# Performance work log

Hardware: AMD Instinct MI355X
Metric: run time of the kernel (lower is better)

Reference implementation:

```python
import jax, jax.numpy as jnp
import numpy as np

DIM_IN = 1024
DIM_OUT = 1024
BATCH = 4
SEQ = 2048


def setup_inputs() -> dict:
    key = jax.random.key(0)
    kx, kq, kk, kv = jax.random.split(key, 4)
    scale = 1.0 / np.sqrt(DIM_IN)
    x = jax.random.normal(kx, (BATCH, SEQ, DIM_IN), dtype=jnp.float32)
    # Weights stored as [dim_in, dim_out] (transpose of torch Linear's [out, in]);
    # y = x @ W is equivalent math to torch's x @ W_t.T
    Wq = jax.random.normal(kq, (DIM_IN, DIM_OUT), dtype=jnp.float32) * scale
    Wk = jax.random.normal(kk, (DIM_IN, DIM_OUT), dtype=jnp.float32) * scale
    Wv = jax.random.normal(kv, (DIM_IN, DIM_OUT), dtype=jnp.float32) * scale
    return {"x": x, "Wq": Wq, "Wk": Wk, "Wv": Wv}


def reference(x, Wq, Wk, Wv):
    # x: [b, s, d_in]; single-head causal self-attention (dropout=0 -> identity)
    q = jnp.einsum("bsd,de->bse", x, Wq)
    k = jnp.einsum("bsd,de->bse", x, Wk)
    v = jnp.einsum("bsd,de->bse", x, Wv)
    dim_k = k.shape[-1]
    scores = jnp.einsum("bqe,bke->bqk", q, k) / jnp.sqrt(jnp.float32(dim_k))
    s = x.shape[1]
    causal = jnp.tril(jnp.ones((s, s), dtype=bool))  # True = keep
    scores = jnp.where(causal[None, :, :], scores, -jnp.inf)
    weights = jax.nn.softmax(scores, axis=-1)
    context = jnp.einsum("bqk,bke->bqe", weights, v)
    return context
```

## Files before the change

### kernel.cpp

```cpp
#include <hip/hip_runtime.h>
#include <cstdint>
#include <cstddef>

typedef unsigned short u16;
typedef __bf16 bf16x8 __attribute__((ext_vector_type(8)));
typedef float f32x4 __attribute__((ext_vector_type(4)));

__device__ inline u16 f2b(float f) {
    uint32_t u = __builtin_bit_cast(uint32_t, f);
    u += 0x7FFFu + ((u >> 16) & 1u);
    return (u16)(u >> 16);
}

__device__ inline void gl2lds16(const u16* g, u16* l) {
    __builtin_amdgcn_global_load_lds(
        (const __attribute__((address_space(1))) void*)g,
        (__attribute__((address_space(3))) void*)l, 16, 0, 0);
}

__global__ void convert_x_kernel(const float* __restrict__ x, u16* __restrict__ xb) {
    size_t i = ((size_t)blockIdx.x * 256 + threadIdx.x) * 4;
    float4 v = *(const float4*)(x + i);
    uint2 pack;
    pack.x = (uint32_t)f2b(v.x) | ((uint32_t)f2b(v.y) << 16);
    pack.y = (uint32_t)f2b(v.z) | ((uint32_t)f2b(v.w) << 16);
    *(uint2*)(xb + i) = pack;
}

__global__ void transpose_w_kernel(const float* __restrict__ Wq,
                                   const float* __restrict__ Wk,
                                   const float* __restrict__ Wv,
                                   u16* __restrict__ QKWT, u16* __restrict__ WvT) {
    __shared__ u16 t[32][33];
    const int z = blockIdx.z;
    const float* W = (z == 0) ? Wq : ((z == 1) ? Wk : Wv);
    u16* dst = (z == 0) ? QKWT : ((z == 1) ? QKWT + 1024 * 1024 : WvT);
    const float scale = (z == 0) ? 0.03125f : 1.0f;
    const int bx = blockIdx.x * 32;
    const int by = blockIdx.y * 32;
    const int tx = threadIdx.x, ty = threadIdx.y;
    #pragma unroll
    for (int r = 0; r < 32; r += 8)
        t[ty + r][tx] = f2b(W[(size_t)(by + ty + r) * 1024 + bx + tx] * scale);
    __syncthreads();
    #pragma unroll
    for (int r = 0; r < 32; r += 8)
        dst[(size_t)(bx + ty + r) * 1024 + (by + tx)] = t[tx][ty + r];
}

template<int EPI>
__device__ __forceinline__ void gemm_body(
    u16* __restrict__ smem,
    const u16* __restrict__ A, int lda,
    const u16* __restrict__ B, int ldb,
    char* __restrict__ Cb, int ldc,
    int m0, int n0, int Kloc, float* __restrict__ lrow) {
    constexpr int BK = 32;
    const int tid = threadIdx.x;
    const int lane = tid & 63, wave = tid >> 6;
    const int wm = wave >> 1, wn = wave & 1;
    const int fl = lane & 15, fh = lane >> 4;

    const int q0 = wave * 2;
    const int srow = lane >> 2, skoff = (lane & 3) * 8;
    const u16* ApL0 = A + (size_t)(m0 + q0 * 16 + srow) * lda + skoff;
    const u16* ApL1 = ApL0 + (size_t)16 * lda;
    const u16* BpL0 = B + (size_t)(n0 + q0 * 16 + srow) * ldb + skoff;
    const u16* BpL1 = BpL0 + (size_t)16 * ldb;

    u16* const Ab[2] = { smem, smem + 4096 };
    u16* const Bb[2] = { smem + 8192, smem + 12288 };

    auto issue = [&](int buf, int k0) {
        gl2lds16(ApL0 + k0, Ab[buf] + q0 * 512);
        gl2lds16(ApL1 + k0, Ab[buf] + q0 * 512 + 512);
        gl2lds16(BpL0 + k0, Bb[buf] + q0 * 512);
        gl2lds16(BpL1 + k0, Bb[buf] + q0 * 512 + 512);
    };

    const f32x4 vzero = {0.f, 0.f, 0.f, 0.f};
    f32x4 acc[4][4];
    #pragma unroll
    for (int i = 0; i < 4; ++i)
        #pragma unroll
        for (int j = 0; j < 4; ++j) acc[i][j] = vzero;

    issue(0, 0);
    int buf = 0;
    for (int k0 = 0; k0 < Kloc; k0 += BK, buf ^= 1) {
        __syncthreads();
        if (k0 + BK < Kloc) issue(buf ^ 1, k0 + BK);
        bf16x8 af[4], bfr[4];
        #pragma unroll
        for (int t = 0; t < 4; ++t) {
            af[t]  = *(const bf16x8*)&Ab[buf][(wm * 64 + t * 16 + fl) * BK + fh * 8];
            bfr[t] = *(const bf16x8*)&Bb[buf][(wn * 64 + t * 16 + fl) * BK + fh * 8];
        }
        #pragma unroll
        for (int mt = 0; mt < 4; ++mt)
            #pragma unroll
            for (int nt = 0; nt < 4; ++nt)
                acc[mt][nt] = __builtin_amdgcn_mfma_f32_16x16x32_bf16(
                    af[mt], bfr[nt], acc[mt][nt], 0, 0, 0);
    }

    if (EPI == 0) {
        u16* Cp = (u16*)Cb;
        #pragma unroll
        for (int mt = 0; mt < 4; ++mt)
            #pragma unroll
            for (int nt = 0; nt < 4; ++nt)
                #pragma unroll
                for (int r = 0; r < 4; ++r) {
                    int row = m0 + wm * 64 + mt * 16 + fh * 4 + r;
                    int col = n0 + wn * 64 + nt * 16 + fl;
                    Cp[(size_t)row * ldc + col] = f2b(acc[mt][nt][r]);
                }
    } else if (EPI == 2) {
        u16* Cp = (u16*)Cb;
        #pragma unroll
        for (int mt = 0; mt < 4; ++mt)
            #pragma unroll
            for (int r = 0; r < 4; ++r) {
                int row = m0 + wm * 64 + mt * 16 + fh * 4 + r;
                float part = 0.f;
                #pragma unroll
                for (int nt = 0; nt < 4; ++nt) {
                    int col = n0 + wn * 64 + nt * 16 + fl;
                    float p = (col <= row) ? __expf(acc[mt][nt][r]) : 0.f;
                    part += p;
                    Cp[(size_t)row * ldc + col] = f2b(p);
                }
                #pragma unroll
                for (int off = 1; off < 16; off <<= 1)
                    part += __shfl_xor(part, off, 64);
                if (fl == 0) atomicAdd(lrow + row, part);
            }
    } else {
        float* Cp = (float*)Cb;
        #pragma unroll
        for (int mt = 0; mt < 4; ++mt)
            #pragma unroll
            for (int r = 0; r < 4; ++r) {
                int row = m0 + wm * 64 + mt * 16 + fh * 4 + r;
                float inv = 1.0f / lrow[row];
                #pragma unroll
                for (int nt = 0; nt < 4; ++nt) {
                    int col = n0 + wn * 64 + nt * 16 + fl;
                    Cp[(size_t)row * ldc + col] = acc[mt][nt][r] * inv;
                }
            }
    }
}

__global__ __launch_bounds__(256)
void proj_kernel(const u16* __restrict__ xb, const u16* __restrict__ QKWT,
                 const u16* __restrict__ WvT, u16* __restrict__ QK,
                 u16* __restrict__ Vt) {
    __shared__ __align__(16) u16 smem[16384];
    int bid = blockIdx.x;
    const u16 *A, *B;
    char* C;
    int lda, ldb, ldc, m0, n0;
    if (bid < 1024) {
        int jt = bid & 15, it = bid >> 4;
        A = xb;  lda = 1024;  B = QKWT;  ldb = 1024;
        C = (char*)QK;  ldc = 2048;  m0 = it * 128;  n0 = jt * 128;
    } else {
        int b = bid - 1024;
        int jt = b & 63, it = b >> 6;
        A = WvT;  lda = 1024;  B = xb;  ldb = 1024;
        C = (char*)Vt;  ldc = 8192;  m0 = it * 128;  n0 = jt * 128;
    }
    gemm_body<0>(smem, A, lda, B, ldb, C, ldc, m0, n0, 1024, nullptr);
}

__global__ __launch_bounds__(256)
void scores_kernel(const u16* __restrict__ QK, u16* __restrict__ P,
                   float* __restrict__ l) {
    __shared__ __align__(16) u16 smem[16384];
    const int t = blockIdx.x, z = blockIdx.y;
    int it = (int)((sqrtf(8.0f * t + 1.0f) - 1.0f) * 0.5f);
    while ((it + 1) * (it + 2) / 2 <= t) ++it;
    while (it * (it + 1) / 2 > t) --it;
    const int jt = t - it * (it + 1) / 2;
    const u16* Qz = QK + (size_t)z * 2048 * 2048;
    const u16* Kz = Qz + 1024;
    u16* Pz = P + (size_t)z * 2048 * 2048;
    gemm_body<2>(smem, Qz, 2048, Kz, 2048, (char*)Pz, 2048,
                 it * 128, jt * 128, 1024, l + (size_t)z * 2048);
}

__global__ __launch_bounds__(256)
void out_kernel(const u16* __restrict__ P, const u16* __restrict__ Vt,
                float* __restrict__ out, float* __restrict__ l) {
    __shared__ __align__(16) u16 smem[16384];
    const int jt = blockIdx.x;
    const int it = 15 - (int)blockIdx.y;
    const int z = blockIdx.z;
    gemm_body<3>(smem, P + (size_t)z * 2048 * 2048, 2048,
                 Vt + (size_t)z * 2048, 8192,
                 (char*)(out + (size_t)z * 2048 * 1024), 1024,
                 it * 128, jt * 128, (it + 1) * 128, l + (size_t)z * 2048);
}

extern "C" void kernel_launch(void* const* d_in, const int* in_sizes, int n_in,
                              void* d_out, int out_size, void* d_ws, size_t ws_size,
                              hipStream_t stream) {
    (void)in_sizes; (void)n_in; (void)out_size; (void)ws_size;
    const float* x  = (const float*)d_in[0];
    const float* Wq = (const float*)d_in[1];
    const float* Wk = (const float*)d_in[2];
    const float* Wv = (const float*)d_in[3];
    float* out = (float*)d_out;

    const size_t MB = 1u << 20;
    char* ws = (char*)d_ws;
    u16* xb   = (u16*)(ws);
    u16* QKWT = (u16*)(ws + 16 * MB);
    u16* WvT  = (u16*)(ws + 20 * MB);
    u16* QK   = (u16*)(ws + 22 * MB);
    u16* Vt   = (u16*)(ws + 54 * MB);
    u16* P    = (u16*)(ws + 70 * MB);
    float* l  = (float*)(ws + 102 * MB);

    hipMemsetAsync(l, 0, 8192 * sizeof(float), stream);
    convert_x_kernel<<<8192, 256, 0, stream>>>(x, xb);
    transpose_w_kernel<<<dim3(32, 32, 3), dim3(32, 8), 0, stream>>>(Wq, Wk, Wv, QKWT, WvT);

    proj_kernel<<<1536, 256, 0, stream>>>(xb, QKWT, WvT, QK, Vt);
    scores_kernel<<<dim3(136, 4), 256, 0, stream>>>(QK, P, l);
    out_kernel<<<dim3(8, 16, 4), 256, 0, stream>>>(P, Vt, out, l);
}
```

Measured before the change: 257.6 us.

## Replace LDS-staged GEMM tiles with direct register-prefetched global loads

The shared GEMM body stops staging A/B tiles through LDS with global_load_lds double buffering and barriers. Each wave now loads its MFMA fragments straight from global memory into registers, software-pipelined two K-steps deep, and launch bounds request 3 blocks per SM. This removes LDS traffic and __syncthreads, but gives up data sharing across waves: each tile is fetched twice from global/L2, and register pressure rises. Out_kernel's K length, (it+1)*128, is a multiple of 64, so the unrolled-by-64 loop stays valid.

Measured after the change: 483.2 us. 87.6% more time.

```diff
diff --git a/kernel.cpp b/kernel.cpp
--- a/kernel.cpp
+++ b/kernel.cpp
@@ -10,12 +10,6 @@
     uint32_t u = __builtin_bit_cast(uint32_t, f);
     u += 0x7FFFu + ((u >> 16) & 1u);
     return (u16)(u >> 16);
-}
-
-__device__ inline void gl2lds16(const u16* g, u16* l) {
-    __builtin_amdgcn_global_load_lds(
-        (const __attribute__((address_space(1))) void*)g,
-        (__attribute__((address_space(3))) void*)l, 16, 0, 0);
 }
 
 __global__ void convert_x_kernel(const float* __restrict__ x, u16* __restrict__ xb) {
@@ -50,33 +44,19 @@
 
 template<int EPI>
 __device__ __forceinline__ void gemm_body(
-    u16* __restrict__ smem,
     const u16* __restrict__ A, int lda,
     const u16* __restrict__ B, int ldb,
     char* __restrict__ Cb, int ldc,
     int m0, int n0, int Kloc, float* __restrict__ lrow) {
-    constexpr int BK = 32;
     const int tid = threadIdx.x;
     const int lane = tid & 63, wave = tid >> 6;
     const int wm = wave >> 1, wn = wave & 1;
     const int fl = lane & 15, fh = lane >> 4;
 
-    const int q0 = wave * 2;
-    const int srow = lane >> 2, skoff = (lane & 3) * 8;
-    const u16* ApL0 = A + (size_t)(m0 + q0 * 16 + srow) * lda + skoff;
-    const u16* ApL1 = ApL0 + (size_t)16 * lda;
-    const u16* BpL0 = B + (size_t)(n0 + q0 * 16 + srow) * ldb + skoff;
-    const u16* BpL1 = BpL0 + (size_t)16 * ldb;
-
-    u16* const Ab[2] = { smem, smem + 4096 };
-    u16* const Bb[2] = { smem + 8192, smem + 12288 };
-
-    auto issue = [&](int buf, int k0) {
-        gl2lds16(ApL0 + k0, Ab[buf] + q0 * 512);
-        gl2lds16(ApL1 + k0, Ab[buf] + q0 * 512 + 512);
-        gl2lds16(BpL0 + k0, Bb[buf] + q0 * 512);
-        gl2lds16(BpL1 + k0, Bb[buf] + q0 * 512 + 512);
-    };
+    const u16* Ap = A + (size_t)(m0 + wm * 64 + fl) * lda + fh * 8;
+    const u16* Bp = B + (size_t)(n0 + wn * 64 + fl) * ldb + fh * 8;
+    const size_t sA = (size_t)16 * lda;
+    const size_t sB = (size_t)16 * ldb;
 
     const f32x4 vzero = {0.f, 0.f, 0.f, 0.f};
     f32x4 acc[4][4];
@@ -85,23 +65,39 @@
         #pragma unroll
         for (int j = 0; j < 4; ++j) acc[i][j] = vzero;
 
-    issue(0, 0);
-    int buf = 0;
-    for (int k0 = 0; k0 < Kloc; k0 += BK, buf ^= 1) {
-        __syncthreads();
-        if (k0 + BK < Kloc) issue(buf ^ 1, k0 + BK);
-        bf16x8 af[4], bfr[4];
+    bf16x8 a0[4], b0[4], a1[4], b1[4];
+
+    #pragma unroll
+    for (int t = 0; t < 4; ++t) {
+        a0[t] = *(const bf16x8*)(Ap + t * sA);
+        b0[t] = *(const bf16x8*)(Bp + t * sB);
+    }
+
+    for (int k0 = 0; k0 < Kloc; k0 += 64) {
         #pragma unroll
         for (int t = 0; t < 4; ++t) {
-            af[t]  = *(const bf16x8*)&Ab[buf][(wm * 64 + t * 16 + fl) * BK + fh * 8];
-            bfr[t] = *(const bf16x8*)&Bb[buf][(wn * 64 + t * 16 + fl) * BK + fh * 8];
+            a1[t] = *(const bf16x8*)(Ap + t * sA + k0 + 32);
+            b1[t] = *(const bf16x8*)(Bp + t * sB + k0 + 32);
         }
         #pragma unroll
         for (int mt = 0; mt < 4; ++mt)
             #pragma unroll
             for (int nt = 0; nt < 4; ++nt)
                 acc[mt][nt] = __builtin_amdgcn_mfma_f32_16x16x32_bf16(
-                    af[mt], bfr[nt], acc[mt][nt], 0, 0, 0);
+                    a0[mt], b0[nt], acc[mt][nt], 0, 0, 0);
+        if (k0 + 64 < Kloc) {
+            #pragma unroll
+            for (int t = 0; t < 4; ++t) {
+                a0[t] = *(const bf16x8*)(Ap + t * sA + k0 + 64);
+                b0[t] = *(const bf16x8*)(Bp + t * sB + k0 + 64);
+            }
+        }
+        #pragma unroll
+        for (int mt = 0; mt < 4; ++mt)
+            #pragma unroll
+            for (int nt = 0; nt < 4; ++nt)
+                acc[mt][nt] = __builtin_amdgcn_mfma_f32_16x16x32_bf16(
+                    a1[mt], b1[nt], acc[mt][nt], 0, 0, 0);
     }
 
     if (EPI == 0) {
@@ -153,32 +149,26 @@
     }
 }
 
-__global__ __launch_bounds__(256)
+__global__ __launch_bounds__(256, 3)
 void proj_kernel(const u16* __restrict__ xb, const u16* __restrict__ QKWT,
                  const u16* __restrict__ WvT, u16* __restrict__ QK,
                  u16* __restrict__ Vt) {
-    __shared__ __align__(16) u16 smem[16384];
     int bid = blockIdx.x;
-    const u16 *A, *B;
-    char* C;
-    int lda, ldb, ldc, m0, n0;
     if (bid < 1024) {
         int jt = bid & 15, it = bid >> 4;
-        A = xb;  lda = 1024;  B = QKWT;  ldb = 1024;
-        C = (char*)QK;  ldc = 2048;  m0 = it * 128;  n0 = jt * 128;
+        gemm_body<0>(xb, 1024, QKWT, 1024, (char*)QK, 2048,
+                     it * 128, jt * 128, 1024, nullptr);
     } else {
         int b = bid - 1024;
         int jt = b & 63, it = b >> 6;
-        A = WvT;  lda = 1024;  B = xb;  ldb = 1024;
-        C = (char*)Vt;  ldc = 8192;  m0 = it * 128;  n0 = jt * 128;
-    }
-    gemm_body<0>(smem, A, lda, B, ldb, C, ldc, m0, n0, 1024, nullptr);
-}
-
-__global__ __launch_bounds__(256)
+        gemm_body<0>(WvT, 1024, xb, 1024, (char*)Vt, 8192,
+                     it * 128, jt * 128, 1024, nullptr);
+    }
+}
+
+__global__ __launch_bounds__(256, 3)
 void scores_kernel(const u16* __restrict__ QK, u16* __restrict__ P,
                    float* __restrict__ l) {
-    __shared__ __align__(16) u16 smem[16384];
     const int t = blockIdx.x, z = blockIdx.y;
     int it = (int)((sqrtf(8.0f * t + 1.0f) - 1.0f) * 0.5f);
     while ((it + 1) * (it + 2) / 2 <= t) ++it;
@@ -187,18 +177,17 @@
     const u16* Qz = QK + (size_t)z * 2048 * 2048;
     const u16* Kz = Qz + 1024;
     u16* Pz = P + (size_t)z * 2048 * 2048;
-    gemm_body<2>(smem, Qz, 2048, Kz, 2048, (char*)Pz, 2048,
+    gemm_body<2>(Qz, 2048, Kz, 2048, (char*)Pz, 2048,
                  it * 128, jt * 128, 1024, l + (size_t)z * 2048);
 }
 
-__global__ __launch_bounds__(256)
+__global__ __launch_bounds__(256, 3)
 void out_kernel(const u16* __restrict__ P, const u16* __restrict__ Vt,
                 float* __restrict__ out, float* __restrict__ l) {
-    __shared__ __align__(16) u16 smem[16384];
     const int jt = blockIdx.x;
     const int it = 15 - (int)blockIdx.y;
     const int z = blockIdx.z;
-    gemm_body<3>(smem, P + (size_t)z * 2048 * 2048, 2048,
+    gemm_body<3>(P + (size_t)z * 2048 * 2048, 2048,
                  Vt + (size_t)z * 2048, 8192,
                  (char*)(out + (size_t)z * 2048 * 1024), 1024,
                  it * 128, jt * 128, (it + 1) * 128, l + (size_t)z * 2048);
```

## Split-K long causal rows in output GEMM, swizzle LDS, fuse prep kernels

Applied to the files above, without the earlier changes.

Splits the K dimension of the heaviest causal row tiles of the P·V GEMM into two blocks that accumulate via float atomics, balancing work across blocks; the output is zeroed with a memset first. Adds an XOR swizzle to the LDS layout of the GEMM tiles to reduce bank conflicts on fragment reads. Merges the x conversion and weight transpose kernels into a single launch. Costs include an extra output memset and atomic traffic on half the output rows, and nondeterministic summation order.

After: 266.1 us. 1.03x slower.

```diff
diff --git a/kernel.cpp b/kernel.cpp
--- a/kernel.cpp
+++ b/kernel.cpp
@@ -18,27 +18,31 @@
         (__attribute__((address_space(3))) void*)l, 16, 0, 0);
 }
 
-__global__ void convert_x_kernel(const float* __restrict__ x, u16* __restrict__ xb) {
-    size_t i = ((size_t)blockIdx.x * 256 + threadIdx.x) * 4;
-    float4 v = *(const float4*)(x + i);
-    uint2 pack;
-    pack.x = (uint32_t)f2b(v.x) | ((uint32_t)f2b(v.y) << 16);
-    pack.y = (uint32_t)f2b(v.z) | ((uint32_t)f2b(v.w) << 16);
-    *(uint2*)(xb + i) = pack;
-}
-
-__global__ void transpose_w_kernel(const float* __restrict__ Wq,
-                                   const float* __restrict__ Wk,
-                                   const float* __restrict__ Wv,
-                                   u16* __restrict__ QKWT, u16* __restrict__ WvT) {
+__global__ void prep_kernel(const float* __restrict__ x, u16* __restrict__ xb,
+                            const float* __restrict__ Wq,
+                            const float* __restrict__ Wk,
+                            const float* __restrict__ Wv,
+                            u16* __restrict__ QKWT, u16* __restrict__ WvT) {
     __shared__ u16 t[32][33];
-    const int z = blockIdx.z;
+    const int bid = blockIdx.x;
+    if (bid < 8192) {
+        size_t i = ((size_t)bid * 256 + threadIdx.x) * 4;
+        float4 v = *(const float4*)(x + i);
+        uint2 pack;
+        pack.x = (uint32_t)f2b(v.x) | ((uint32_t)f2b(v.y) << 16);
+        pack.y = (uint32_t)f2b(v.z) | ((uint32_t)f2b(v.w) << 16);
+        *(uint2*)(xb + i) = pack;
+        return;
+    }
+    const int tb = bid - 8192;
+    const int z = tb >> 10;
+    const int rem = tb & 1023;
+    const int by = (rem >> 5) * 32;
+    const int bx = (rem & 31) * 32;
     const float* W = (z == 0) ? Wq : ((z == 1) ? Wk : Wv);
     u16* dst = (z == 0) ? QKWT : ((z == 1) ? QKWT + 1024 * 1024 : WvT);
     const float scale = (z == 0) ? 0.03125f : 1.0f;
-    const int bx = blockIdx.x * 32;
-    const int by = blockIdx.y * 32;
-    const int tx = threadIdx.x, ty = threadIdx.y;
+    const int tx = threadIdx.x & 31, ty = threadIdx.x >> 5;
     #pragma unroll
     for (int r = 0; r < 32; r += 8)
         t[ty + r][tx] = f2b(W[(size_t)(by + ty + r) * 1024 + bx + tx] * scale);
@@ -54,7 +58,7 @@
     const u16* __restrict__ A, int lda,
     const u16* __restrict__ B, int ldb,
     char* __restrict__ Cb, int ldc,
-    int m0, int n0, int Kloc, float* __restrict__ lrow) {
+    int m0, int n0, int Kloc, float* __restrict__ lrow, bool split = false) {
     constexpr int BK = 32;
     const int tid = threadIdx.x;
     const int lane = tid & 63, wave = tid >> 6;
@@ -62,7 +66,8 @@
     const int fl = lane & 15, fh = lane >> 4;
 
     const int q0 = wave * 2;
-    const int srow = lane >> 2, skoff = (lane & 3) * 8;
+    const int srow = lane >> 2;
+    const int skoff = ((lane & 3) ^ ((lane >> 3) & 3)) * 8;
     const u16* ApL0 = A + (size_t)(m0 + q0 * 16 + srow) * lda + skoff;
     const u16* ApL1 = ApL0 + (size_t)16 * lda;
     const u16* BpL0 = B + (size_t)(n0 + q0 * 16 + srow) * ldb + skoff;
@@ -85,6 +90,8 @@
         #pragma unroll
         for (int j = 0; j < 4; ++j) acc[i][j] = vzero;
 
+    const int rcx = (fl >> 1) & 3;
+
     issue(0, 0);
     int buf = 0;
     for (int k0 = 0; k0 < Kloc; k0 += BK, buf ^= 1) {
@@ -93,8 +100,8 @@
         bf16x8 af[4], bfr[4];
         #pragma unroll
         for (int t = 0; t < 4; ++t) {
-            af[t]  = *(const bf16x8*)&Ab[buf][(wm * 64 + t * 16 + fl) * BK + fh * 8];
-            bfr[t] = *(const bf16x8*)&Bb[buf][(wn * 64 + t * 16 + fl) * BK + fh * 8];
+            af[t]  = *(const bf16x8*)&Ab[buf][(wm * 64 + t * 16 + fl) * BK + (fh ^ rcx) * 8];
+            bfr[t] = *(const bf16x8*)&Bb[buf][(wn * 64 + t * 16 + fl) * BK + (fh ^ rcx) * 8];
         }
         #pragma unroll
         for (int mt = 0; mt < 4; ++mt)
@@ -147,7 +154,9 @@
                 #pragma unroll
                 for (int nt = 0; nt < 4; ++nt) {
                     int col = n0 + wn * 64 + nt * 16 + fl;
-                    Cp[(size_t)row * ldc + col] = acc[mt][nt][r] * inv;
+                    float v = acc[mt][nt][r] * inv;
+                    if (split) atomicAdd(&Cp[(size_t)row * ldc + col], v);
+                    else       Cp[(size_t)row * ldc + col] = v;
                 }
             }
     }
@@ -159,20 +168,16 @@
                  u16* __restrict__ Vt) {
     __shared__ __align__(16) u16 smem[16384];
     int bid = blockIdx.x;
-    const u16 *A, *B;
-    char* C;
-    int lda, ldb, ldc, m0, n0;
     if (bid < 1024) {
         int jt = bid & 15, it = bid >> 4;
-        A = xb;  lda = 1024;  B = QKWT;  ldb = 1024;
-        C = (char*)QK;  ldc = 2048;  m0 = it * 128;  n0 = jt * 128;
+        gemm_body<0>(smem, xb, 1024, QKWT, 1024, (char*)QK, 2048,
+                     it * 128, jt * 128, 1024, nullptr);
     } else {
         int b = bid - 1024;
         int jt = b & 63, it = b >> 6;
-        A = WvT;  lda = 1024;  B = xb;  ldb = 1024;
-        C = (char*)Vt;  ldc = 8192;  m0 = it * 128;  n0 = jt * 128;
-    }
-    gemm_body<0>(smem, A, lda, B, ldb, C, ldc, m0, n0, 1024, nullptr);
+        gemm_body<0>(smem, WvT, 1024, xb, 1024, (char*)Vt, 8192,
+                     it * 128, jt * 128, 1024, nullptr);
+    }
 }
 
 __global__ __launch_bounds__(256)
@@ -195,19 +200,30 @@
 void out_kernel(const u16* __restrict__ P, const u16* __restrict__ Vt,
                 float* __restrict__ out, float* __restrict__ l) {
     __shared__ __align__(16) u16 smem[16384];
-    const int jt = blockIdx.x;
-    const int it = 15 - (int)blockIdx.y;
-    const int z = blockIdx.z;
-    gemm_body<3>(smem, P + (size_t)z * 2048 * 2048, 2048,
-                 Vt + (size_t)z * 2048, 8192,
+    const int jt = blockIdx.x, c = blockIdx.y, z = blockIdx.z;
+    int it, k0, kloc;
+    bool split;
+    if (c < 16) {
+        it = 8 + (c >> 1);
+        kloc = (it + 1) * 64;
+        k0 = (c & 1) * kloc;
+        split = true;
+    } else {
+        it = c - 16;
+        k0 = 0;
+        kloc = (it + 1) * 128;
+        split = false;
+    }
+    gemm_body<3>(smem, P + (size_t)z * 2048 * 2048 + k0, 2048,
+                 Vt + (size_t)z * 2048 + k0, 8192,
                  (char*)(out + (size_t)z * 2048 * 1024), 1024,
-                 it * 128, jt * 128, (it + 1) * 128, l + (size_t)z * 2048);
+                 it * 128, jt * 128, kloc, l + (size_t)z * 2048, split);
 }
 
 extern "C" void kernel_launch(void* const* d_in, const int* in_sizes, int n_in,
                               void* d_out, int out_size, void* d_ws, size_t ws_size,
                               hipStream_t stream) {
-    (void)in_sizes; (void)n_in; (void)out_size; (void)ws_size;
+    (void)in_sizes; (void)n_in; (void)ws_size;
     const float* x  = (const float*)d_in[0];
     const float* Wq = (const float*)d_in[1];
     const float* Wk = (const float*)d_in[2];
@@ -225,10 +241,10 @@
     float* l  = (float*)(ws + 102 * MB);
 
     hipMemsetAsync(l, 0, 8192 * sizeof(float), stream);
-    convert_x_kernel<<<8192, 256, 0, stream>>>(x, xb);
-    transpose_w_kernel<<<dim3(32, 32, 3), dim3(32, 8), 0, stream>>>(Wq, Wk, Wv, QKWT, WvT);
+    hipMemsetAsync(out, 0, (size_t)out_size * sizeof(float), stream);
+    prep_kernel<<<8192 + 3072, 256, 0, stream>>>(x, xb, Wq, Wk, Wv, QKWT, WvT);
 
     proj_kernel<<<1536, 256, 0, stream>>>(xb, QKWT, WvT, QK, Vt);
     scores_kernel<<<dim3(136, 4), 256, 0, stream>>>(QK, P, l);
-    out_kernel<<<dim3(8, 16, 4), 256, 0, stream>>>(P, Vt, out, l);
-}
+    out_kernel<<<dim3(8, 24, 4), 256, 0, stream>>>(P, Vt, out, l);
+}
```
